# Optimization experiments

Measured on AMD Instinct MI355X. Metric: run time of the kernel, lower is better.

Reference implementation:

```python
import jax, jax.numpy as jnp
import numpy as np

B, C, HID, H, W = 8, 256, 256, 128, 128


def setup_inputs() -> dict:
    key = jax.random.key(0)
    ks = jax.random.split(key, 8)
    x = jax.random.normal(ks[0], (B, C, H, W), dtype=jnp.float32)
    prior = jax.random.normal(ks[1], (B, 1, H, W), dtype=jnp.float32)
    # xavier-uniform-style 1x1 conv weights: limit = sqrt(6/(fan_in+fan_out))
    lim_i = float(np.sqrt(6.0 / (C + HID)))
    lim_o = float(np.sqrt(6.0 / (HID + C)))
    Wi = jax.random.uniform(ks[2], (HID, C), minval=-lim_i, maxval=lim_i, dtype=jnp.float32)
    bi = jnp.zeros((HID,), dtype=jnp.float32)
    Wo = jax.random.uniform(ks[3], (C, HID), minval=-lim_o, maxval=lim_o, dtype=jnp.float32)
    bo = jnp.zeros((C,), dtype=jnp.float32)
    A_param = 0.1 * jax.random.normal(ks[4], (HID,), dtype=jnp.float32)
    B_param = 0.1 * jax.random.normal(ks[5], (HID,), dtype=jnp.float32)
    alpha = jnp.asarray(0.1, dtype=jnp.float32)
    gamma = jnp.asarray(0.1, dtype=jnp.float32)
    return {"x": x, "prior": prior, "Wi": Wi, "bi": bi, "A_param": A_param,
            "B_param": B_param, "alpha": alpha, "gamma": gamma, "Wo": Wo, "bo": bo}


def _lin_scan(u, a):
    """Linear recurrence h_t = a*h_{t-1} + u_t over leading axis.
    u: [T, B, Ch, X]; a: [Ch]."""
    a_b = a[None, :, None]  # broadcast over [B, Ch, X]
    def step(h, ut):
        h = a_b * h + ut
        return h, h
    _, hs = jax.lax.scan(step, jnp.zeros_like(u[0]), u)
    return hs  # [T, B, Ch, X]


def reference(x, prior, Wi, bi, A_param, B_param, alpha, gamma, Wo, bo):
    # prior is [B,1,H,W] at matching resolution -> only clamp applies
    p = jnp.clip(prior, -1.0, 1.0)
    F_mod = x + alpha * p  # broadcast over channel dim == expand
    # 1x1 conv input projection
    xp = jnp.einsum('bchw,oc->bohw', F_mod, Wi) + bi[None, :, None, None]
    A = jnp.tanh(A_param)
    u = B_param[None, :, None, None] * xp  # B*x term precomputed
    # horizontal recurrence (over width)
    uh = jnp.moveaxis(u, 3, 0)                       # [W,B,Ch,H]
    h_h = jnp.moveaxis(_lin_scan(uh, A), 0, 3)       # [B,Ch,H,W]
    # vertical recurrence (over height)
    uv = jnp.moveaxis(u, 2, 0)                       # [H,B,Ch,W]
    h_v = jnp.moveaxis(_lin_scan(uv, A), 0, 2)       # [B,Ch,H,W]
    h_fused = h_h + h_v
    out = jnp.einsum('bchw,oc->bohw', h_fused, Wo) + bo[None, :, None, None]
    return F_mod + gamma * out
```

## Files before the change

### kernel.cpp

```cpp
#include <hip/hip_runtime.h>
#include <hip/hip_bf16.h>


typedef unsigned int u32;
typedef unsigned short u16;
typedef __bf16 bf16x8 __attribute__((ext_vector_type(8)));
typedef float f32x4 __attribute__((ext_vector_type(4)));

__device__ __forceinline__ float bf2f(u16 r) { return __uint_as_float(((u32)r) << 16); }
__device__ __forceinline__ u16 f2bf(float f) {
    u32 x = __float_as_uint(f);
    return (u16)((x + 0x7FFFu + ((x >> 16) & 1u)) >> 16);
}
__device__ __forceinline__ float clip1(float v) { return fminf(1.f, fmaxf(-1.f, v)); }

__device__ __forceinline__ void gload16(const void* g, void* l) {
    __builtin_amdgcn_global_load_lds((__attribute__((address_space(1))) void*)g,
                                     (__attribute__((address_space(3))) void*)l, 16, 0, 0);
}

__global__ __launch_bounds__(256) void kw_conv(const float* __restrict__ Wi,
                                               const float* __restrict__ Wo,
                                               u16* __restrict__ Wib, u16* __restrict__ Wob) {
    int i = blockIdx.x * 256 + threadIdx.x;
    Wib[i] = f2bf(Wi[i]);
    Wob[i] = f2bf(Wo[i]);
}

__global__ __launch_bounds__(256) void k0_transpose(const float* __restrict__ x,
                                                    const float* __restrict__ prior,
                                                    const float* __restrict__ alpha_p,
                                                    u16* __restrict__ Fb) {
    __shared__ u16 tile[64][68];
    const int t = threadIdx.x;
    const int bx = blockIdx.x;
    const int b = bx >> 10, cb = (bx >> 8) & 3, pb = bx & 255;
    const int c0 = cb * 64, p0 = pb * 64;
    const float alpha = alpha_p[0];
    const int lp = (t & 15) * 4;
    const int rr = t >> 4;
#pragma unroll
    for (int r = 0; r < 4; ++r) {
        const int c = r * 16 + rr;
        const float4 xv = *(const float4*)&x[((size_t)(b * 256 + c0 + c)) * 16384 + p0 + lp];
        const float4 pv = *(const float4*)&prior[(size_t)b * 16384 + p0 + lp];
        ushort4 fv;
        fv.x = f2bf(xv.x + alpha * clip1(pv.x));
        fv.y = f2bf(xv.y + alpha * clip1(pv.y));
        fv.z = f2bf(xv.z + alpha * clip1(pv.z));
        fv.w = f2bf(xv.w + alpha * clip1(pv.w));
        *(ushort4*)&tile[c][lp] = fv;
    }
    __syncthreads();
#pragma unroll
    for (int r = 0; r < 4; ++r) {
        const int p = r * 16 + rr;
        ushort4 v;
        v.x = tile[lp + 0][p];
        v.y = tile[lp + 1][p];
        v.z = tile[lp + 2][p];
        v.w = tile[lp + 3][p];
        *(ushort4*)&Fb[((size_t)b * 16384 + p0 + p) * 256 + c0 + lp] = v;
    }
}

__global__ __launch_bounds__(512) void k1_gemm1(const u16* __restrict__ Fb,
                                                const u16* __restrict__ Wib,
                                                const float* __restrict__ bi,
                                                const float* __restrict__ Bp,
                                                u16* __restrict__ u) {
    __shared__ __align__(16) u16 sA[2][128 * 32];
    __shared__ __align__(16) u16 sB[2][256 * 32];
    const int t = threadIdx.x;
    const int bx = blockIdx.x;
    const int b = bx >> 7, mt = bx & 127;
    const size_t Fbase = ((size_t)b * 16384 + (size_t)mt * 128) * 256;
    const int wave = t >> 6, l = t & 63;
    const int wr = wave >> 2, wc = wave & 3;
    const int lr = l & 15, lg = l >> 4;

    f32x4 acc[4][4];
#pragma unroll
    for (int mi = 0; mi < 4; ++mi)
#pragma unroll
        for (int ni = 0; ni < 4; ++ni) acc[mi][ni] = (f32x4){0.f, 0.f, 0.f, 0.f};

#define STAGE1(buf, ks)                                                                  \
    do {                                                                                 \
        const int k0_ = (ks) * 32;                                                       \
        { const int s = t;                                                               \
          gload16(&Fb[Fbase + (size_t)(s >> 2) * 256 + k0_ + (s & 3) * 8],               \
                  &sA[buf][s * 8]); }                                                    \
        { const int s = t;                                                               \
          gload16(&Wib[(size_t)(s >> 2) * 256 + k0_ + (s & 3) * 8], &sB[buf][s * 8]); }  \
        { const int s = t + 512;                                                         \
          gload16(&Wib[(size_t)(s >> 2) * 256 + k0_ + (s & 3) * 8], &sB[buf][s * 8]); }  \
    } while (0)

    int cur = 0;
    STAGE1(0, 0);
    __syncthreads();
    for (int ks = 0; ks < 8; ++ks) {
        if (ks < 7) STAGE1(cur ^ 1, ks + 1);
        bf16x8 af[4], bfv[4];
#pragma unroll
        for (int mi = 0; mi < 4; ++mi)
            af[mi] = *(const bf16x8*)&sA[cur][(wr * 64 + mi * 16 + lr) * 32 + lg * 8];
#pragma unroll
        for (int ni = 0; ni < 4; ++ni)
            bfv[ni] = *(const bf16x8*)&sB[cur][(wc * 64 + ni * 16 + lr) * 32 + lg * 8];
#pragma unroll
        for (int mi = 0; mi < 4; ++mi)
#pragma unroll
            for (int ni = 0; ni < 4; ++ni)
                acc[mi][ni] =
                    __builtin_amdgcn_mfma_f32_16x16x32_bf16(af[mi], bfv[ni], acc[mi][ni], 0, 0, 0);
        __syncthreads();
        cur ^= 1;
    }
#undef STAGE1

    float bp4[4], bi4[4];
#pragma unroll
    for (int ni = 0; ni < 4; ++ni) {
        const int o = wc * 64 + ni * 16 + lr;
        bp4[ni] = Bp[o];
        bi4[ni] = bi[o];
    }
    u16* ub = u + ((size_t)b * 16384 + (size_t)mt * 128) * 256;
#pragma unroll
    for (int mi = 0; mi < 4; ++mi)
#pragma unroll
        for (int j = 0; j < 4; ++j) {
            const int p_loc = wr * 64 + mi * 16 + lg * 4 + j;
            u16* row = ub + (size_t)p_loc * 256;
#pragma unroll
            for (int ni = 0; ni < 4; ++ni) {
                const int o = wc * 64 + ni * 16 + lr;
                row[o] = f2bf(bp4[ni] * (acc[mi][ni][j] + bi4[ni]));
            }
        }
}

__global__ __launch_bounds__(256) void k2h(const u16* __restrict__ u, u16* __restrict__ hh,
                                           const float* __restrict__ A_param) {
    const int o = threadIdx.x;
    const float A = tanhf(A_param[o]);
    size_t base = (size_t)blockIdx.x * (128 * 256) + o;
    float hacc = 0.f;
    for (int wb = 0; wb < 16; ++wb) {
        float v[8];
#pragma unroll
        for (int j = 0; j < 8; ++j) v[j] = bf2f(u[base + (size_t)j * 256]);
        u16 w8[8];
#pragma unroll
        for (int j = 0; j < 8; ++j) {
            hacc = fmaf(A, hacc, v[j]);
            w8[j] = f2bf(hacc);
        }
#pragma unroll
        for (int j = 0; j < 8; ++j) hh[base + (size_t)j * 256] = w8[j];
        base += 8 * 256;
    }
}

__global__ __launch_bounds__(256) void k2v(u16* __restrict__ u, const u16* __restrict__ hh,
                                           const float* __restrict__ A_param) {
    const int o = threadIdx.x;
    const int b = blockIdx.x >> 7, w = blockIdx.x & 127;
    const float A = tanhf(A_param[o]);
    size_t base = ((size_t)b * 16384 + w) * 256 + o;
    float hacc = 0.f;
    for (int hb = 0; hb < 16; ++hb) {
        float v[8], g[8];
#pragma unroll
        for (int j = 0; j < 8; ++j) {
            v[j] = bf2f(u[base + (size_t)j * 32768]);
            g[j] = bf2f(hh[base + (size_t)j * 32768]);
        }
        u16 w8[8];
#pragma unroll
        for (int j = 0; j < 8; ++j) {
            hacc = fmaf(A, hacc, v[j]);
            w8[j] = f2bf(hacc + g[j]);
        }
#pragma unroll
        for (int j = 0; j < 8; ++j) u[base + (size_t)j * 32768] = w8[j];
        base += (size_t)8 * 32768;
    }
}

__global__ __launch_bounds__(512) void k3_gemm2(const u16* __restrict__ hf,
                                                const u16* __restrict__ Wob,
                                                const float* __restrict__ x,
                                                const float* __restrict__ prior,
                                                const float* __restrict__ bo,
                                                const float* __restrict__ alpha_p,
                                                const float* __restrict__ gamma_p,
                                                float* __restrict__ out) {
    __shared__ __align__(16) u16 sA[2][256 * 32];
    __shared__ __align__(16) u16 sB[2][128 * 32];
    const int t = threadIdx.x;
    const int bx = blockIdx.x;
    const int b = bx >> 7, nt = bx & 127;
    const size_t Hbase = ((size_t)b * 16384 + (size_t)nt * 128) * 256;
    const int wave = t >> 6, l = t & 63;
    const int wr = wave >> 1, wc = wave & 1;
    const int lr = l & 15, lg = l >> 4;

    f32x4 acc[4][4];
#pragma unroll
    for (int mi = 0; mi < 4; ++mi)
#pragma unroll
        for (int ni = 0; ni < 4; ++ni) acc[mi][ni] = (f32x4){0.f, 0.f, 0.f, 0.f};

#define STAGE3(buf, ks)                                                                   \
    do {                                                                                  \
        const int k0_ = (ks) * 32;                                                        \
        { const int s = t;                                                                \
          gload16(&Wob[(size_t)(s >> 2) * 256 + k0_ + (s & 3) * 8], &sA[buf][s * 8]); }   \
        { const int s = t + 512;                                                          \
          gload16(&Wob[(size_t)(s >> 2) * 256 + k0_ + (s & 3) * 8], &sA[buf][s * 8]); }   \
        { const int s = t;                                                                \
          gload16(&hf[Hbase + (size_t)(s >> 2) * 256 + k0_ + (s & 3) * 8],                \
                  &sB[buf][s * 8]); }                                                     \
    } while (0)

    int cur = 0;
    STAGE3(0, 0);
    __syncthreads();
    for (int ks = 0; ks < 8; ++ks) {
        if (ks < 7) STAGE3(cur ^ 1, ks + 1);
        bf16x8 af[4], bfv[4];
#pragma unroll
        for (int mi = 0; mi < 4; ++mi)
            af[mi] = *(const bf16x8*)&sA[cur][(wr * 64 + mi * 16 + lr) * 32 + lg * 8];
#pragma unroll
        for (int ni = 0; ni < 4; ++ni)
            bfv[ni] = *(const bf16x8*)&sB[cur][(wc * 64 + ni * 16 + lr) * 32 + lg * 8];
#pragma unroll
        for (int mi = 0; mi < 4; ++mi)
#pragma unroll
            for (int ni = 0; ni < 4; ++ni)
                acc[mi][ni] =
                    __builtin_amdgcn_mfma_f32_16x16x32_bf16(af[mi], bfv[ni], acc[mi][ni], 0, 0, 0);
        __syncthreads();
        cur ^= 1;
    }
#undef STAGE3

    const float alpha = alpha_p[0], gamma = gamma_p[0];
    float pr4[4];
#pragma unroll
    for (int ni = 0; ni < 4; ++ni) {
        const int p_loc = wc * 64 + ni * 16 + lr;
        pr4[ni] = clip1(prior[(size_t)b * 16384 + (size_t)nt * 128 + p_loc]);
    }
#pragma unroll
    for (int mi = 0; mi < 4; ++mi)
#pragma unroll
        for (int j = 0; j < 4; ++j) {
            const int o = wr * 64 + mi * 16 + lg * 4 + j;
            const float bov = bo[o];
            const size_t obase = ((size_t)b * 256 + o) * 16384 + (size_t)nt * 128;
#pragma unroll
            for (int ni = 0; ni < 4; ++ni) {
                const int p_loc = wc * 64 + ni * 16 + lr;
                out[obase + p_loc] =
                    x[obase + p_loc] + alpha * pr4[ni] + gamma * (acc[mi][ni][j] + bov);
            }
        }
}

extern "C" void kernel_launch(void* const* d_in, const int* in_sizes, int n_in,
                              void* d_out, int out_size, void* d_ws, size_t ws_size,
                              hipStream_t stream) {
    const float* x = (const float*)d_in[0];
    const float* prior = (const float*)d_in[1];
    const float* Wi = (const float*)d_in[2];
    const float* bi = (const float*)d_in[3];
    const float* A_param = (const float*)d_in[4];
    const float* B_param = (const float*)d_in[5];
    const float* alpha = (const float*)d_in[6];
    const float* gamma = (const float*)d_in[7];
    const float* Wo = (const float*)d_in[8];
    const float* bo = (const float*)d_in[9];
    float* out = (float*)d_out;

    u16* u = (u16*)d_ws;
    u16* Fb = (u16*)((char*)d_ws + 67108864ull);
    u16* hh = Fb;
    u16* Wib = (u16*)((char*)d_ws + 134217728ull);
    u16* Wob = (u16*)((char*)d_ws + 134348800ull);

    hipLaunchKernelGGL(kw_conv, dim3(256), dim3(256), 0, stream, Wi, Wo, Wib, Wob);
    hipLaunchKernelGGL(k0_transpose, dim3(8192), dim3(256), 0, stream, x, prior, alpha, Fb);
    hipLaunchKernelGGL(k1_gemm1, dim3(1024), dim3(512), 0, stream, Fb, Wib, bi, B_param, u);
    hipLaunchKernelGGL(k2h, dim3(1024), dim3(256), 0, stream, u, hh, A_param);
    hipLaunchKernelGGL(k2v, dim3(1024), dim3(256), 0, stream, u, hh, A_param);
    hipLaunchKernelGGL(k3_gemm2, dim3(1024), dim3(512), 0, stream, u, Wob, x, prior, bo, alpha,
                       gamma, out);
}
```

Before: 198.5 us.

## Fuse input transpose and horizontal scan into the first projection GEMM

The separate transpose/convert kernel and horizontal-scan kernel are removed. Each GEMM1 block now covers one image row: it reads x in NCHW directly, adds the clipped prior, converts to bf16 into a padded LDS tile, and after the MMA loop stages the projected row in LDS. Half the waves then run the width recurrence from LDS and write hh, while the other half copy u to global. This drops the Fb intermediate round trip and the reread of u for the horizontal scan, at the cost of strided scalar LDS writes, more LDS per block, and a serial scan tail that uses only half the threads.

```diff
diff --git a/kernel.cpp b/kernel.cpp
--- a/kernel.cpp
+++ b/kernel.cpp
@@ -1,5 +1,6 @@
 #include <hip/hip_runtime.h>
 #include <hip/hip_bf16.h>
+#include <math.h>
 
 
 typedef unsigned int u32;
@@ -27,98 +28,109 @@
     Wob[i] = f2bf(Wo[i]);
 }
 
-__global__ __launch_bounds__(256) void k0_transpose(const float* __restrict__ x,
-                                                    const float* __restrict__ prior,
-                                                    const float* __restrict__ alpha_p,
-                                                    u16* __restrict__ Fb) {
-    __shared__ u16 tile[64][68];
+#define SA_STRIDE 40
+__global__ __launch_bounds__(512) void k01_gemm1(const float* __restrict__ x,
+                                                 const float* __restrict__ prior,
+                                                 const u16* __restrict__ Wib,
+                                                 const float* __restrict__ bi,
+                                                 const float* __restrict__ Bp,
+                                                 const float* __restrict__ A_param,
+                                                 const float* __restrict__ alpha_p,
+                                                 u16* __restrict__ u, u16* __restrict__ hh) {
+    __shared__ __align__(16) char smem[65536];
+    u16* sA = (u16*)smem;
+    u16* sB = (u16*)(smem + 20480);
+    u16* ut = (u16*)smem;
+
     const int t = threadIdx.x;
-    const int bx = blockIdx.x;
-    const int b = bx >> 10, cb = (bx >> 8) & 3, pb = bx & 255;
-    const int c0 = cb * 64, p0 = pb * 64;
-    const float alpha = alpha_p[0];
-    const int lp = (t & 15) * 4;
-    const int rr = t >> 4;
-#pragma unroll
-    for (int r = 0; r < 4; ++r) {
-        const int c = r * 16 + rr;
-        const float4 xv = *(const float4*)&x[((size_t)(b * 256 + c0 + c)) * 16384 + p0 + lp];
-        const float4 pv = *(const float4*)&prior[(size_t)b * 16384 + p0 + lp];
-        ushort4 fv;
-        fv.x = f2bf(xv.x + alpha * clip1(pv.x));
-        fv.y = f2bf(xv.y + alpha * clip1(pv.y));
-        fv.z = f2bf(xv.z + alpha * clip1(pv.z));
-        fv.w = f2bf(xv.w + alpha * clip1(pv.w));
-        *(ushort4*)&tile[c][lp] = fv;
-    }
-    __syncthreads();
-#pragma unroll
-    for (int r = 0; r < 4; ++r) {
-        const int p = r * 16 + rr;
-        ushort4 v;
-        v.x = tile[lp + 0][p];
-        v.y = tile[lp + 1][p];
-        v.z = tile[lp + 2][p];
-        v.w = tile[lp + 3][p];
-        *(ushort4*)&Fb[((size_t)b * 16384 + p0 + p) * 256 + c0 + lp] = v;
-    }
-}
-
-__global__ __launch_bounds__(512) void k1_gemm1(const u16* __restrict__ Fb,
-                                                const u16* __restrict__ Wib,
-                                                const float* __restrict__ bi,
-                                                const float* __restrict__ Bp,
-                                                u16* __restrict__ u) {
-    __shared__ __align__(16) u16 sA[2][128 * 32];
-    __shared__ __align__(16) u16 sB[2][256 * 32];
-    const int t = threadIdx.x;
-    const int bx = blockIdx.x;
-    const int b = bx >> 7, mt = bx & 127;
-    const size_t Fbase = ((size_t)b * 16384 + (size_t)mt * 128) * 256;
+    const int b = blockIdx.x >> 7, h = blockIdx.x & 127;
     const int wave = t >> 6, l = t & 63;
     const int wr = wave >> 2, wc = wave & 3;
     const int lr = l & 15, lg = l >> 4;
 
+    const int cl = t & 31, w0 = (t >> 5) * 8;
+    const float alpha = alpha_p[0];
+
+    const float* prow = prior + (size_t)b * 16384 + h * 128 + w0;
+    float fp[8];
+    {
+        float4 p0 = *(const float4*)prow;
+        float4 p1 = *(const float4*)(prow + 4);
+        fp[0] = alpha * clip1(p0.x); fp[1] = alpha * clip1(p0.y);
+        fp[2] = alpha * clip1(p0.z); fp[3] = alpha * clip1(p0.w);
+        fp[4] = alpha * clip1(p1.x); fp[5] = alpha * clip1(p1.y);
+        fp[6] = alpha * clip1(p1.z); fp[7] = alpha * clip1(p1.w);
+    }
+    const float* xrow = x + ((size_t)b * 256 * 128 + h) * 128;
+
     f32x4 acc[4][4];
 #pragma unroll
     for (int mi = 0; mi < 4; ++mi)
 #pragma unroll
         for (int ni = 0; ni < 4; ++ni) acc[mi][ni] = (f32x4){0.f, 0.f, 0.f, 0.f};
 
-#define STAGE1(buf, ks)                                                                  \
-    do {                                                                                 \
-        const int k0_ = (ks) * 32;                                                       \
-        { const int s = t;                                                               \
-          gload16(&Fb[Fbase + (size_t)(s >> 2) * 256 + k0_ + (s & 3) * 8],               \
-                  &sA[buf][s * 8]); }                                                    \
-        { const int s = t;                                                               \
-          gload16(&Wib[(size_t)(s >> 2) * 256 + k0_ + (s & 3) * 8], &sB[buf][s * 8]); }  \
-        { const int s = t + 512;                                                         \
-          gload16(&Wib[(size_t)(s >> 2) * 256 + k0_ + (s & 3) * 8], &sB[buf][s * 8]); }  \
+    float4 xa, xb;
+#define LOADX(ks)                                                        \
+    do {                                                                 \
+        const float* p_ = xrow + (size_t)((ks) * 32 + cl) * 16384 + w0;  \
+        xa = *(const float4*)p_;                                         \
+        xb = *(const float4*)(p_ + 4);                                   \
     } while (0)
+#define CVTWR(buf)                                            \
+    do {                                                      \
+        u16* d_ = sA + (buf) * (128 * SA_STRIDE);             \
+        d_[(w0 + 0) * SA_STRIDE + cl] = f2bf(xa.x + fp[0]);   \
+        d_[(w0 + 1) * SA_STRIDE + cl] = f2bf(xa.y + fp[1]);   \
+        d_[(w0 + 2) * SA_STRIDE + cl] = f2bf(xa.z + fp[2]);   \
+        d_[(w0 + 3) * SA_STRIDE + cl] = f2bf(xa.w + fp[3]);   \
+        d_[(w0 + 4) * SA_STRIDE + cl] = f2bf(xb.x + fp[4]);   \
+        d_[(w0 + 5) * SA_STRIDE + cl] = f2bf(xb.y + fp[5]);   \
+        d_[(w0 + 6) * SA_STRIDE + cl] = f2bf(xb.z + fp[6]);   \
+        d_[(w0 + 7) * SA_STRIDE + cl] = f2bf(xb.w + fp[7]);   \
+    } while (0)
+#define STAGEB(buf, ks)                                                                     \
+    do {                                                                                    \
+        const int k0_ = (ks) * 32;                                                          \
+        { const int s = t;                                                                  \
+          gload16(&Wib[(size_t)(s >> 2) * 256 + k0_ + (s & 3) * 8],                         \
+                  sB + (buf) * 8192 + s * 8); }                                             \
+        { const int s = t + 512;                                                            \
+          gload16(&Wib[(size_t)(s >> 2) * 256 + k0_ + (s & 3) * 8],                         \
+                  sB + (buf) * 8192 + s * 8); }                                             \
+    } while (0)
+
+    LOADX(0);
+    STAGEB(0, 0);
+    CVTWR(0);
+    __syncthreads();
 
     int cur = 0;
-    STAGE1(0, 0);
-    __syncthreads();
     for (int ks = 0; ks < 8; ++ks) {
-        if (ks < 7) STAGE1(cur ^ 1, ks + 1);
+        if (ks < 7) {
+            LOADX(ks + 1);
+            STAGEB(cur ^ 1, ks + 1);
+        }
         bf16x8 af[4], bfv[4];
 #pragma unroll
         for (int mi = 0; mi < 4; ++mi)
-            af[mi] = *(const bf16x8*)&sA[cur][(wr * 64 + mi * 16 + lr) * 32 + lg * 8];
+            af[mi] = *(const bf16x8*)&sA[cur * (128 * SA_STRIDE) +
+                                         (wr * 64 + mi * 16 + lr) * SA_STRIDE + lg * 8];
 #pragma unroll
         for (int ni = 0; ni < 4; ++ni)
-            bfv[ni] = *(const bf16x8*)&sB[cur][(wc * 64 + ni * 16 + lr) * 32 + lg * 8];
+            bfv[ni] = *(const bf16x8*)&sB[cur * 8192 + (wc * 64 + ni * 16 + lr) * 32 + lg * 8];
 #pragma unroll
         for (int mi = 0; mi < 4; ++mi)
 #pragma unroll
             for (int ni = 0; ni < 4; ++ni)
                 acc[mi][ni] =
                     __builtin_amdgcn_mfma_f32_16x16x32_bf16(af[mi], bfv[ni], acc[mi][ni], 0, 0, 0);
+        if (ks < 7) CVTWR(cur ^ 1);
         __syncthreads();
         cur ^= 1;
     }
-#undef STAGE1
+#undef LOADX
+#undef CVTWR
+#undef STAGEB
 
     float bp4[4], bi4[4];
 #pragma unroll
@@ -127,40 +139,46 @@
         bp4[ni] = Bp[o];
         bi4[ni] = bi[o];
     }
-    u16* ub = u + ((size_t)b * 16384 + (size_t)mt * 128) * 256;
 #pragma unroll
     for (int mi = 0; mi < 4; ++mi)
 #pragma unroll
         for (int j = 0; j < 4; ++j) {
-            const int p_loc = wr * 64 + mi * 16 + lg * 4 + j;
-            u16* row = ub + (size_t)p_loc * 256;
+            const int w = wr * 64 + mi * 16 + lg * 4 + j;
 #pragma unroll
             for (int ni = 0; ni < 4; ++ni) {
                 const int o = wc * 64 + ni * 16 + lr;
-                row[o] = f2bf(bp4[ni] * (acc[mi][ni][j] + bi4[ni]));
+                ut[w * 256 + o] = f2bf(bp4[ni] * (acc[mi][ni][j] + bi4[ni]));
             }
         }
-}
-
-__global__ __launch_bounds__(256) void k2h(const u16* __restrict__ u, u16* __restrict__ hh,
-                                           const float* __restrict__ A_param) {
-    const int o = threadIdx.x;
-    const float A = tanhf(A_param[o]);
-    size_t base = (size_t)blockIdx.x * (128 * 256) + o;
-    float hacc = 0.f;
-    for (int wb = 0; wb < 16; ++wb) {
-        float v[8];
-#pragma unroll
-        for (int j = 0; j < 8; ++j) v[j] = bf2f(u[base + (size_t)j * 256]);
-        u16 w8[8];
-#pragma unroll
-        for (int j = 0; j < 8; ++j) {
-            hacc = fmaf(A, hacc, v[j]);
-            w8[j] = f2bf(hacc);
-        }
-#pragma unroll
-        for (int j = 0; j < 8; ++j) hh[base + (size_t)j * 256] = w8[j];
-        base += 8 * 256;
+    __syncthreads();
+
+    const size_t gbase = ((size_t)b * 16384 + (size_t)h * 128) * 256;
+    if (wave < 4) {
+        const int o = t;
+        const float A = tanhf(A_param[o]);
+        float hacc = 0.f;
+        for (int wb = 0; wb < 16; ++wb) {
+            float v[8];
+#pragma unroll
+            for (int j = 0; j < 8; ++j) v[j] = bf2f(ut[(wb * 8 + j) * 256 + o]);
+            u16 s8[8];
+#pragma unroll
+            for (int j = 0; j < 8; ++j) {
+                hacc = fmaf(A, hacc, v[j]);
+                s8[j] = f2bf(hacc);
+            }
+#pragma unroll
+            for (int j = 0; j < 8; ++j) hh[gbase + (size_t)(wb * 8 + j) * 256 + o] = s8[j];
+        }
+    } else {
+        const int t2 = t - 256;
+        int4* ug = (int4*)(u + gbase);
+        const int4* us = (const int4*)ut;
+#pragma unroll
+        for (int i = 0; i < 16; ++i) {
+            const int chunk = t2 + 256 * i;
+            ug[chunk] = us[chunk];
+        }
     }
 }
 
@@ -288,15 +306,13 @@
     float* out = (float*)d_out;
 
     u16* u = (u16*)d_ws;
-    u16* Fb = (u16*)((char*)d_ws + 67108864ull);
-    u16* hh = Fb;
+    u16* hh = (u16*)((char*)d_ws + 67108864ull);
     u16* Wib = (u16*)((char*)d_ws + 134217728ull);
     u16* Wob = (u16*)((char*)d_ws + 134348800ull);
 
     hipLaunchKernelGGL(kw_conv, dim3(256), dim3(256), 0, stream, Wi, Wo, Wib, Wob);
-    hipLaunchKernelGGL(k0_transpose, dim3(8192), dim3(256), 0, stream, x, prior, alpha, Fb);
-    hipLaunchKernelGGL(k1_gemm1, dim3(1024), dim3(512), 0, stream, Fb, Wib, bi, B_param, u);
-    hipLaunchKernelGGL(k2h, dim3(1024), dim3(256), 0, stream, u, hh, A_param);
+    hipLaunchKernelGGL(k01_gemm1, dim3(1024), dim3(512), 0, stream, x, prior, Wib, bi, B_param,
+                       A_param, alpha, u, hh);
     hipLaunchKernelGGL(k2v, dim3(1024), dim3(256), 0, stream, u, hh, A_param);
     hipLaunchKernelGGL(k3_gemm2, dim3(1024), dim3(512), 0, stream, u, Wob, x, prior, bo, alpha,
                        gamma, out);
```

Result: faster. 174.7 us (median of 2 runs) (-12.0%).
